# Kernel tuning notes

Hardware: AMD Instinct MI355X
Metric: run time of the kernel (lower is better)

## Reference

```python
import jax, jax.numpy as jnp
import numpy as np

B, N = 2, 512
D_NODE, D_EDGE, D_HID, H = 128, 64, 128, 8
DH = D_HID // H  # per-head dim = 16
SCALE = 1.0 / (D_HID ** 0.5)  # note: scale uses full d_hid as in source


def setup_inputs() -> dict:
    key = jax.random.key(0)
    k1, k2, k3, k4 = jax.random.split(key, 4)
    node_features = jax.random.normal(k1, (B, N, D_NODE), dtype=jnp.float32)
    edge_features = jax.random.normal(k2, (B, N, N, D_EDGE), dtype=jnp.float32)
    mask = jnp.ones((B, N, N), dtype=bool)
    # Linear weights (stored as (in, out); math identical to torch x @ W.T)
    W_node = jax.random.normal(k3, (D_NODE, 3 * D_HID), dtype=jnp.float32) / np.sqrt(D_NODE)
    W_edge = jax.random.normal(k4, (D_EDGE, 3 * D_HID), dtype=jnp.float32) / np.sqrt(D_EDGE)
    return {"node_features": node_features, "edge_features": edge_features,
            "mask": mask, "W_node": W_node, "W_edge": W_edge}


def _split_heads_node(x):
    # (b, n, h*c) -> (b, h, n, c)
    b, n, hc = x.shape
    return x.reshape(b, n, H, hc // H).transpose(0, 2, 1, 3)


def _split_heads_edge(x):
    # (b, n, m, h*c) -> (b, h, n, m, c)
    b, n, m, hc = x.shape
    return x.reshape(b, n, m, H, hc // H).transpose(0, 3, 1, 2, 4)


def reference(node_features, edge_features, mask, W_node, W_edge):
    # node qkv: (b, n, 3*d_hid) -> (b, h, n, 3*dh) -> chunk
    qkv_n = _split_heads_node(node_features @ W_node)
    q_node, k_node, v_node = jnp.split(qkv_n, 3, axis=-1)  # each (b,h,n,dh)
    # edge qkv: (b, n, n, 3*d_hid) -> (b, h, n, n, 3*dh) -> chunk
    qkv_e = _split_heads_edge(edge_features @ W_edge)
    q_edge, k_edge, v_edge = jnp.split(qkv_e, 3, axis=-1)  # each (b,h,n,n,dh)

    q = q_node[:, :, :, None, :] + q_edge   # (b,h,i,j,dh)
    k = k_node[:, :, None, :, :] + k_edge   # (b,h,i,j,dh)
    v = v_node[:, :, None, :, :] + v_edge   # (b,h,i,j,dh)

    dots = SCALE * jnp.einsum('bhijd,bhijd->bhij', q, k)
    attn = jax.nn.softmax(dots, axis=-1)
    out = jnp.einsum('bhij,bhijd->bhid', attn, v)  # (b,h,n,dh)
    # (b,h,n,dh) -> (b,n,h*dh)
    b, h, n, dh = out.shape
    return out.transpose(0, 2, 1, 3).reshape(b, n, h * dh)
```

## Files before the change

### kernel.cpp

```cpp
#include <hip/hip_runtime.h>

#define NN 512
#define OC 384
#define S2F 0.12751694f

typedef __attribute__((ext_vector_type(8))) short short8;
typedef __attribute__((ext_vector_type(4))) float f32x4;

__device__ __forceinline__ unsigned short f2bf(float x) {
    unsigned u = __builtin_bit_cast(unsigned, x);
    u = (u + 0x7fffu + ((u >> 16) & 1u)) >> 16;
    return (unsigned short)u;
}

__global__ __launch_bounds__(256) void prep0_kernel(
    const float* __restrict__ Wn, const float* __restrict__ We,
    const float* __restrict__ node,
    unsigned short* __restrict__ WtN, unsigned short* __restrict__ WtE,
    unsigned short* __restrict__ nodeBf)
{
    int idx = blockIdx.x * 256 + threadIdx.x;
    if (idx < 24576) {
        int o = idx >> 6, k = idx & 63;
        WtE[idx] = f2bf(We[k * OC + o]);
    } else if (idx < 24576 + 49152) {
        int id = idx - 24576;
        int o = id >> 7, k = id & 127;
        WtN[id] = f2bf(Wn[k * OC + o]);
    } else {
        int id = idx - 73728;
        nodeBf[id] = f2bf(node[id]);
    }
}

__global__ __launch_bounds__(256) void prep1_kernel(
    const unsigned short* __restrict__ nodeBf,
    const unsigned short* __restrict__ WtN,
    float* __restrict__ qnF,
    float* __restrict__ nodeKV)
{
    const int t = threadIdx.x;
    const int w = t >> 6;
    const int lane = t & 63;
    const int lj = lane & 15;
    const int quad = lane >> 4;
    const int nbase = blockIdx.x * 32;

    short8 bfr[2][4];
#pragma unroll
    for (int nt = 0; nt < 2; ++nt)
#pragma unroll
        for (int ks = 0; ks < 4; ++ks)
            bfr[nt][ks] = *reinterpret_cast<const short8*>(
                nodeBf + (size_t)(nbase + nt * 16 + lj) * 128 + ks * 32 + quad * 8);

#pragma unroll
    for (int m = 0; m < 6; ++m) {
        int ot = (6 * w + m) * 16;
        short8 afr[4];
#pragma unroll
        for (int ks = 0; ks < 4; ++ks)
            afr[ks] = *reinterpret_cast<const short8*>(
                WtN + (size_t)(ot + lj) * 128 + ks * 32 + quad * 8);
#pragma unroll
        for (int nt = 0; nt < 2; ++nt) {
            f32x4 acc = {0.f, 0.f, 0.f, 0.f};
#pragma unroll
            for (int ks = 0; ks < 4; ++ks)
                acc = __builtin_amdgcn_mfma_f32_16x16x32_bf16(afr[ks], bfr[nt][ks], acc, 0, 0, 0);
            int n = nbase + nt * 16 + lj;
            int bb = n >> 9, ii = n & 511;
#pragma unroll
            for (int r = 0; r < 4; ++r) {
                int o = ot + quad * 4 + r;
                int h = o / 48, rem = o - h * 48;
                size_t base = (size_t)(bb * 8 + h) * NN + ii;
                if (rem < 16) {
                    qnF[base * 16 + rem] = acc[r];
                } else {
                    int d = (rem - 16) & 15;
                    int isv = (rem >= 32) ? 4 : 0;
                    nodeKV[base * 32 + (d >> 2) * 8 + isv + (d & 3)] = acc[r];
                }
            }
        }
    }
}

__global__ __launch_bounds__(512, 4) void rt_attn_main(
    const float* __restrict__ edge,
    const float* __restrict__ qnF,
    const float* __restrict__ nodeKV,
    const unsigned short* __restrict__ WtE,
    float* __restrict__ out)
{
    __shared__ unsigned short sE[2][64 * 72];
    __shared__ float sRed[8][256];
    const int bi = blockIdx.x;
    const int b = bi >> 9;
    const int i = bi & 511;
    const int t = threadIdx.x;
    const int h = t >> 6;
    const int lane = t & 63;
    const int lj = lane & 15;
    const int quad = lane >> 4;

    const int sj0 = t >> 4;
    const int sj1 = sj0 + 32;
    const int sc = (t & 15) * 4;

    short8 afr[3][2];
#pragma unroll
    for (int T = 0; T < 3; ++T)
#pragma unroll
        for (int sec = 0; sec < 2; ++sec)
            afr[T][sec] = *reinterpret_cast<const short8*>(
                WtE + (size_t)(h * 48 + T * 16 + lj) * 64 + sec * 32 + quad * 8);

    const f32x4 qn = *reinterpret_cast<const f32x4*>(
        qnF + ((size_t)(b * 8 + h) * NN + i) * 16 + quad * 4);

    float l = 0.f;
    float oa[4] = {0.f, 0.f, 0.f, 0.f};

    const float* eBase = edge + (size_t)bi * NN * 64;
    const float* kvBase = nodeKV + (size_t)(b * 8 + h) * NN * 32;
    float* red = &sRed[h][0];
    const int wb = lj * 4 + quad;
    f32x4 pf0, pf1;

    pf0 = *reinterpret_cast<const f32x4*>(eBase + (size_t)sj0 * 64 + sc);
    pf1 = *reinterpret_cast<const f32x4*>(eBase + (size_t)sj1 * 64 + sc);
    {
        ushort4 u0, u1;
        u0.x = f2bf(pf0[0]); u0.y = f2bf(pf0[1]); u0.z = f2bf(pf0[2]); u0.w = f2bf(pf0[3]);
        u1.x = f2bf(pf1[0]); u1.y = f2bf(pf1[1]); u1.z = f2bf(pf1[2]); u1.w = f2bf(pf1[3]);
        *reinterpret_cast<ushort4*>(&sE[0][sj0 * 72 + sc]) = u0;
        *reinterpret_cast<ushort4*>(&sE[0][sj1 * 72 + sc]) = u1;
    }
    __syncthreads();

    for (int tt = 0; tt < 8; ++tt) {
        const int cur = tt & 1;
        if (tt < 7) {
            const float* nb = eBase + (size_t)(tt + 1) * 4096;
            pf0 = *reinterpret_cast<const f32x4*>(nb + (size_t)sj0 * 64 + sc);
            pf1 = *reinterpret_cast<const f32x4*>(nb + (size_t)sj1 * 64 + sc);
        }
        f32x4 ka[4], va[4];
#pragma unroll
        for (int jn = 0; jn < 4; ++jn) {
            const float* kvp = kvBase + (size_t)(tt * 64 + jn * 16 + lj) * 32 + quad * 8;
            ka[jn] = *reinterpret_cast<const f32x4*>(kvp);
            va[jn] = *reinterpret_cast<const f32x4*>(kvp + 4);
        }
        float dp[4];
#pragma unroll
        for (int jn = 0; jn < 4; ++jn) {
            const int jrow = jn * 16 + lj;
            short8 b0 = *reinterpret_cast<const short8*>(&sE[cur][jrow * 72 + quad * 8]);
            short8 b1 = *reinterpret_cast<const short8*>(&sE[cur][jrow * 72 + 32 + quad * 8]);
            f32x4 fq = qn;
            f32x4 fk = ka[jn];
            fq = __builtin_amdgcn_mfma_f32_16x16x32_bf16(afr[0][0], b0, fq, 0, 0, 0);
            fq = __builtin_amdgcn_mfma_f32_16x16x32_bf16(afr[0][1], b1, fq, 0, 0, 0);
            fk = __builtin_amdgcn_mfma_f32_16x16x32_bf16(afr[1][0], b0, fk, 0, 0, 0);
            fk = __builtin_amdgcn_mfma_f32_16x16x32_bf16(afr[1][1], b1, fk, 0, 0, 0);
            float d0 = fq[0] * fk[0];
            d0 = fmaf(fq[1], fk[1], d0);
            d0 = fmaf(fq[2], fk[2], d0);
            d0 = fmaf(fq[3], fk[3], d0);
            dp[jn] = d0;
        }
        red[wb]       = dp[0];
        red[wb + 64]  = dp[1];
        red[wb + 128] = dp[2];
        red[wb + 192] = dp[3];
        float wg[4];
#pragma unroll
        for (int jn = 0; jn < 4; ++jn) {
            f32x4 s = *reinterpret_cast<const f32x4*>(&red[jn * 64 + lj * 4]);
            wg[jn] = exp2f((s[0] + s[1] + s[2] + s[3]) * S2F);
            l += wg[jn];
        }
        if (tt < 7) {
            ushort4 u0, u1;
            u0.x = f2bf(pf0[0]); u0.y = f2bf(pf0[1]); u0.z = f2bf(pf0[2]); u0.w = f2bf(pf0[3]);
            u1.x = f2bf(pf1[0]); u1.y = f2bf(pf1[1]); u1.z = f2bf(pf1[2]); u1.w = f2bf(pf1[3]);
            *reinterpret_cast<ushort4*>(&sE[cur ^ 1][sj0 * 72 + sc]) = u0;
            *reinterpret_cast<ushort4*>(&sE[cur ^ 1][sj1 * 72 + sc]) = u1;
        }
#pragma unroll
        for (int jn = 0; jn < 4; ++jn) {
            const int jrow = jn * 16 + lj;
            short8 b0 = *reinterpret_cast<const short8*>(&sE[cur][jrow * 72 + quad * 8]);
            short8 b1 = *reinterpret_cast<const short8*>(&sE[cur][jrow * 72 + 32 + quad * 8]);
            f32x4 fv = va[jn];
            fv = __builtin_amdgcn_mfma_f32_16x16x32_bf16(afr[2][0], b0, fv, 0, 0, 0);
            fv = __builtin_amdgcn_mfma_f32_16x16x32_bf16(afr[2][1], b1, fv, 0, 0, 0);
#pragma unroll
            for (int r = 0; r < 4; ++r) oa[r] = fmaf(wg[jn], fv[r], oa[r]);
        }
        if (tt < 7) __syncthreads();
    }

#pragma unroll
    for (int off = 1; off <= 8; off <<= 1) {
        l += __shfl_xor(l, off);
#pragma unroll
        for (int r = 0; r < 4; ++r) oa[r] += __shfl_xor(oa[r], off);
    }
    if (lj == 0) {
        float inv = 1.0f / l;
        f32x4 o4;
#pragma unroll
        for (int r = 0; r < 4; ++r) o4[r] = oa[r] * inv;
        *reinterpret_cast<f32x4*>(out + (size_t)bi * 128 + h * 16 + quad * 4) = o4;
    }
}

extern "C" void kernel_launch(void* const* d_in, const int* in_sizes, int n_in,
                              void* d_out, int out_size, void* d_ws, size_t ws_size,
                              hipStream_t stream) {
    const float* node = (const float*)d_in[0];
    const float* edge = (const float*)d_in[1];
    const float* Wn = (const float*)d_in[3];
    const float* We = (const float*)d_in[4];
    float* out = (float*)d_out;

    char* ws = (char*)d_ws;
    float* qnF = (float*)ws;
    float* nodeKV = (float*)(ws + 524288);
    unsigned short* WtE = (unsigned short*)(ws + 1572864);
    unsigned short* WtN = (unsigned short*)(ws + 1622016);
    unsigned short* nodeBf = (unsigned short*)(ws + 1720320);

    prep0_kernel<<<800, 256, 0, stream>>>(Wn, We, node, WtN, WtE, nodeBf);
    prep1_kernel<<<32, 256, 0, stream>>>(nodeBf, WtN, qnF, nodeKV);
    rt_attn_main<<<2 * NN, 512, 0, stream>>>(edge, qnF, nodeKV, WtE, out);
}
```

Baseline: 254.8 us.

## Split heads across two blocks, replace LDS reduction with shuffles, fuse V MFMA

Each row block is split into two 256-thread blocks, each handling four heads, which doubles the grid. Every block still loads and converts the full 64-wide edge tile, so edge global reads and bf16 conversion work are duplicated. The cross-quad dot-product reduction now uses lane shuffles instead of a shared-memory scratch buffer. The V projection MFMAs are moved into the same loop as Q and K, so the shared-memory B fragments are read once per tile instead of twice.

```diff
diff --git a/kernel.cpp b/kernel.cpp
--- a/kernel.cpp
+++ b/kernel.cpp
@@ -87,7 +87,7 @@
     }
 }
 
-__global__ __launch_bounds__(512, 4) void rt_attn_main(
+__global__ __launch_bounds__(256) void rt_attn_main(
     const float* __restrict__ edge,
     const float* __restrict__ qnF,
     const float* __restrict__ nodeKV,
@@ -95,19 +95,25 @@
     float* __restrict__ out)
 {
     __shared__ unsigned short sE[2][64 * 72];
-    __shared__ float sRed[8][256];
-    const int bi = blockIdx.x;
+    const int blk = blockIdx.x;
+    const int hg = blk & 1;
+    const int bi = blk >> 1;
     const int b = bi >> 9;
     const int i = bi & 511;
     const int t = threadIdx.x;
-    const int h = t >> 6;
+    const int h = hg * 4 + (t >> 6);
     const int lane = t & 63;
     const int lj = lane & 15;
     const int quad = lane >> 4;
 
-    const int sj0 = t >> 4;
-    const int sj1 = sj0 + 32;
+    const int sj[4] = { t >> 4, (256 + t) >> 4, (512 + t) >> 4, (768 + t) >> 4 };
     const int sc = (t & 15) * 4;
+
+    const float* eBase = edge + (size_t)bi * NN * 64;
+    f32x4 pf[4];
+#pragma unroll
+    for (int it = 0; it < 4; ++it)
+        pf[it] = *reinterpret_cast<const f32x4*>(eBase + (size_t)sj[it] * 64 + sc);
 
     short8 afr[3][2];
 #pragma unroll
@@ -122,21 +128,16 @@
 
     float l = 0.f;
     float oa[4] = {0.f, 0.f, 0.f, 0.f};
-
-    const float* eBase = edge + (size_t)bi * NN * 64;
     const float* kvBase = nodeKV + (size_t)(b * 8 + h) * NN * 32;
-    float* red = &sRed[h][0];
-    const int wb = lj * 4 + quad;
-    f32x4 pf0, pf1;
-
-    pf0 = *reinterpret_cast<const f32x4*>(eBase + (size_t)sj0 * 64 + sc);
-    pf1 = *reinterpret_cast<const f32x4*>(eBase + (size_t)sj1 * 64 + sc);
+
     {
-        ushort4 u0, u1;
-        u0.x = f2bf(pf0[0]); u0.y = f2bf(pf0[1]); u0.z = f2bf(pf0[2]); u0.w = f2bf(pf0[3]);
-        u1.x = f2bf(pf1[0]); u1.y = f2bf(pf1[1]); u1.z = f2bf(pf1[2]); u1.w = f2bf(pf1[3]);
-        *reinterpret_cast<ushort4*>(&sE[0][sj0 * 72 + sc]) = u0;
-        *reinterpret_cast<ushort4*>(&sE[0][sj1 * 72 + sc]) = u1;
+#pragma unroll
+        for (int it = 0; it < 4; ++it) {
+            ushort4 u;
+            u.x = f2bf(pf[it][0]); u.y = f2bf(pf[it][1]);
+            u.z = f2bf(pf[it][2]); u.w = f2bf(pf[it][3]);
+            *reinterpret_cast<ushort4*>(&sE[0][sj[it] * 72 + sc]) = u;
+        }
     }
     __syncthreads();
 
@@ -144,8 +145,9 @@
         const int cur = tt & 1;
         if (tt < 7) {
             const float* nb = eBase + (size_t)(tt + 1) * 4096;
-            pf0 = *reinterpret_cast<const f32x4*>(nb + (size_t)sj0 * 64 + sc);
-            pf1 = *reinterpret_cast<const f32x4*>(nb + (size_t)sj1 * 64 + sc);
+#pragma unroll
+            for (int it = 0; it < 4; ++it)
+                pf[it] = *reinterpret_cast<const f32x4*>(nb + (size_t)sj[it] * 64 + sc);
         }
         f32x4 ka[4], va[4];
 #pragma unroll
@@ -155,6 +157,7 @@
             va[jn] = *reinterpret_cast<const f32x4*>(kvp + 4);
         }
         float dp[4];
+        f32x4 fvv[4];
 #pragma unroll
         for (int jn = 0; jn < 4; ++jn) {
             const int jrow = jn * 16 + lj;
@@ -162,45 +165,46 @@
             short8 b1 = *reinterpret_cast<const short8*>(&sE[cur][jrow * 72 + 32 + quad * 8]);
             f32x4 fq = qn;
             f32x4 fk = ka[jn];
+            f32x4 fv = va[jn];
             fq = __builtin_amdgcn_mfma_f32_16x16x32_bf16(afr[0][0], b0, fq, 0, 0, 0);
             fq = __builtin_amdgcn_mfma_f32_16x16x32_bf16(afr[0][1], b1, fq, 0, 0, 0);
             fk = __builtin_amdgcn_mfma_f32_16x16x32_bf16(afr[1][0], b0, fk, 0, 0, 0);
             fk = __builtin_amdgcn_mfma_f32_16x16x32_bf16(afr[1][1], b1, fk, 0, 0, 0);
+            fv = __builtin_amdgcn_mfma_f32_16x16x32_bf16(afr[2][0], b0, fv, 0, 0, 0);
+            fv = __builtin_amdgcn_mfma_f32_16x16x32_bf16(afr[2][1], b1, fv, 0, 0, 0);
+            fvv[jn] = fv;
             float d0 = fq[0] * fk[0];
             d0 = fmaf(fq[1], fk[1], d0);
             d0 = fmaf(fq[2], fk[2], d0);
             d0 = fmaf(fq[3], fk[3], d0);
             dp[jn] = d0;
         }
-        red[wb]       = dp[0];
-        red[wb + 64]  = dp[1];
-        red[wb + 128] = dp[2];
-        red[wb + 192] = dp[3];
-        float wg[4];
+        float t16[4], t32[4], wg[4];
+#pragma unroll
+        for (int jn = 0; jn < 4; ++jn) t16[jn] = __shfl_xor(dp[jn], 16);
+#pragma unroll
+        for (int jn = 0; jn < 4; ++jn) dp[jn] += t16[jn];
+#pragma unroll
+        for (int jn = 0; jn < 4; ++jn) t32[jn] = __shfl_xor(dp[jn], 32);
 #pragma unroll
         for (int jn = 0; jn < 4; ++jn) {
-            f32x4 s = *reinterpret_cast<const f32x4*>(&red[jn * 64 + lj * 4]);
-            wg[jn] = exp2f((s[0] + s[1] + s[2] + s[3]) * S2F);
+            wg[jn] = exp2f((dp[jn] + t32[jn]) * S2F);
             l += wg[jn];
         }
         if (tt < 7) {
-            ushort4 u0, u1;
-            u0.x = f2bf(pf0[0]); u0.y = f2bf(pf0[1]); u0.z = f2bf(pf0[2]); u0.w = f2bf(pf0[3]);
-            u1.x = f2bf(pf1[0]); u1.y = f2bf(pf1[1]); u1.z = f2bf(pf1[2]); u1.w = f2bf(pf1[3]);
-            *reinterpret_cast<ushort4*>(&sE[cur ^ 1][sj0 * 72 + sc]) = u0;
-            *reinterpret_cast<ushort4*>(&sE[cur ^ 1][sj1 * 72 + sc]) = u1;
-        }
-#pragma unroll
-        for (int jn = 0; jn < 4; ++jn) {
-            const int jrow = jn * 16 + lj;
-            short8 b0 = *reinterpret_cast<const short8*>(&sE[cur][jrow * 72 + quad * 8]);
-            short8 b1 = *reinterpret_cast<const short8*>(&sE[cur][jrow * 72 + 32 + quad * 8]);
-            f32x4 fv = va[jn];
-            fv = __builtin_amdgcn_mfma_f32_16x16x32_bf16(afr[2][0], b0, fv, 0, 0, 0);
-            fv = __builtin_amdgcn_mfma_f32_16x16x32_bf16(afr[2][1], b1, fv, 0, 0, 0);
-#pragma unroll
-            for (int r = 0; r < 4; ++r) oa[r] = fmaf(wg[jn], fv[r], oa[r]);
-        }
+#pragma unroll
+            for (int it = 0; it < 4; ++it) {
+                ushort4 u;
+                u.x = f2bf(pf[it][0]); u.y = f2bf(pf[it][1]);
+                u.z = f2bf(pf[it][2]); u.w = f2bf(pf[it][3]);
+                *reinterpret_cast<ushort4*>(&sE[cur ^ 1][sj[it] * 72 + sc]) = u;
+            }
+        }
+#pragma unroll
+        for (int jn = 0; jn < 4; ++jn)
+#pragma unroll
+            for (int r = 0; r < 4; ++r)
+                oa[r] = fmaf(wg[jn], fvv[jn][r], oa[r]);
         if (tt < 7) __syncthreads();
     }
 
@@ -237,5 +241,5 @@
 
     prep0_kernel<<<800, 256, 0, stream>>>(Wn, We, node, WtN, WtE, nodeBf);
     prep1_kernel<<<32, 256, 0, stream>>>(nodeBf, WtN, qnF, nodeKV);
-    rt_attn_main<<<2 * NN, 512, 0, stream>>>(edge, qnF, nodeKV, WtE, out);
-}
+    rt_attn_main<<<2 * 2 * NN, 256, 0, stream>>>(edge, qnF, nodeKV, WtE, out);
+}
```

Result: slower. 267.8 us (+5.1%).
